# Kernel tuning notes

Measured on AMD Instinct MI355X. Metric: run time of the kernel, lower is better.

Reference implementation:

```python
import jax, jax.numpy as jnp
import numpy as np

B, T, D = 4, 2048, 1024  # batch, seq, latent_dim == attn_dim
H = 16                   # n_heads
HS = D // H              # head_size = 64
FF = 4 * D               # ffn hidden
EPS = 1e-5


def layernorm(x, g, b):
    mu = jnp.mean(x, axis=-1, keepdims=True)
    var = jnp.mean(jnp.square(x - mu), axis=-1, keepdims=True)
    return (x - mu) * jax.lax.rsqrt(var + EPS) * g + b


def setup_inputs() -> dict:
    key = jax.random.key(0)
    ks = jax.random.split(key, 12)
    s = lambda fan_in: 1.0 / np.sqrt(fan_in)
    return {
        "x": jax.random.normal(ks[0], (B, T, D), dtype=jnp.float32),
        "ln1_g": jnp.ones((D,), jnp.float32),
        "ln1_b": jnp.zeros((D,), jnp.float32),
        "W_ap": jax.random.normal(ks[1], (D, D), jnp.float32) * s(D),
        "b_ap": jnp.zeros((D,), jnp.float32),
        "W_qkv": jax.random.normal(ks[2], (D, 3 * D), jnp.float32) * s(D),
        "b_qkv": jnp.zeros((3 * D,), jnp.float32),
        "W_proj": jax.random.normal(ks[3], (D, D), jnp.float32) * s(D),
        "b_proj": jnp.zeros((D,), jnp.float32),
        "ln2_g": jnp.ones((D,), jnp.float32),
        "ln2_b": jnp.zeros((D,), jnp.float32),
        "W1": jax.random.normal(ks[4], (D, FF), jnp.float32) * s(D),
        "b1": jnp.zeros((FF,), jnp.float32),
        "W2": jax.random.normal(ks[5], (FF, D), jnp.float32) * s(FF),
        "b2": jnp.zeros((D,), jnp.float32),
    }


def block_fwd(x, ln1_g, ln1_b, W_ap, b_ap, W_qkv, b_qkv, W_proj, b_proj,
              ln2_g, ln2_b, W1, b1, W2, b2):
    # --- self attention branch ---
    a = layernorm(x, ln1_g, ln1_b)
    a = a @ W_ap + b_ap                       # [B,T,D]
    qkv = a @ W_qkv + b_qkv                   # [B,T,3D]
    q, k, v = jnp.split(qkv, 3, axis=-1)
    q = q.reshape(B, T, H, HS).transpose(0, 2, 1, 3)  # [B,H,T,HS]
    k = k.reshape(B, T, H, HS).transpose(0, 2, 1, 3)
    v = v.reshape(B, T, H, HS).transpose(0, 2, 1, 3)
    scores = jnp.einsum('bhqd,bhkd->bhqk', q, k) * (1.0 / np.sqrt(HS))
    probs = jax.nn.softmax(scores, axis=-1)   # full [B,H,T,T], no causal mask (as in source)
    o = jnp.einsum('bhqk,bhkd->bhqd', probs, v)
    o = o.transpose(0, 2, 1, 3).reshape(B, T, D)
    o = o @ W_proj + b_proj
    h = x + o
    # --- ffn branch: GELU(LayerNorm(h)) -> Linear -> GELU -> Linear ---
    f = jax.nn.gelu(layernorm(h, ln2_g, ln2_b), approximate=False)
    f = jax.nn.gelu(f @ W1 + b1, approximate=False) @ W2 + b2
    return h + f


def reference(x, ln1_g, ln1_b, W_ap, b_ap, W_qkv, b_qkv, W_proj, b_proj,
              ln2_g, ln2_b, W1, b1, W2, b2):
    return block_fwd(x, ln1_g, ln1_b, W_ap, b_ap, W_qkv, b_qkv, W_proj, b_proj,
                     ln2_g, ln2_b, W1, b1, W2, b2)
```

## Files before the change

### kernel.cpp

```cpp
#include <hip/hip_runtime.h>
#include <hip/hip_bf16.h>
#include <math.h>


typedef unsigned short u16;
typedef __attribute__((ext_vector_type(8))) short s16x8;
typedef __attribute__((ext_vector_type(4))) float f32x4;

__device__ __forceinline__ u16 f2bf(float f) {
    unsigned u = __float_as_uint(f);
    u += 0x7fffu + ((u >> 16) & 1u);
    return (u16)(u >> 16);
}
__device__ __forceinline__ unsigned pkbf2(float a, float b) {
    float2 t; t.x = a; t.y = b;
    __hip_bfloat162 r = __float22bfloat162_rn(t);
    return *(unsigned*)&r;
}
__device__ __forceinline__ float bf2f(short s) {
    return __uint_as_float(((unsigned)(unsigned short)s) << 16);
}
__device__ __forceinline__ float gelu_f(float v) {
    return 0.5f * v * (1.0f + erff(v * 0.70710678118654752f));
}

__global__ __launch_bounds__(256) void transpose_f32_bf16(
    const float* __restrict__ in, u16* __restrict__ out, int K, int N) {
    __shared__ float t[32][33];
    int n0 = blockIdx.x * 32, k0 = blockIdx.y * 32;
    int c = threadIdx.x, r0 = threadIdx.y;
#pragma unroll
    for (int i = 0; i < 4; i++) {
        int r = r0 + i * 8;
        t[r][c] = in[(size_t)(k0 + r) * N + n0 + c];
    }
    __syncthreads();
#pragma unroll
    for (int i = 0; i < 4; i++) {
        int r = r0 + i * 8;
        out[(size_t)(n0 + r) * K + k0 + c] = f2bf(t[c][r]);
    }
}

template <bool GELU>
__global__ __launch_bounds__(256) void ln_kernel(
    const float* __restrict__ x, const float* __restrict__ g,
    const float* __restrict__ bt, u16* __restrict__ out) {
    const int D = 1024;
    int row = blockIdx.x;
    float4 v = reinterpret_cast<const float4*>(x + (size_t)row * D)[threadIdx.x];
    float s = v.x + v.y + v.z + v.w;
    float s2 = v.x * v.x + v.y * v.y + v.z * v.z + v.w * v.w;
#pragma unroll
    for (int off = 32; off > 0; off >>= 1) {
        s += __shfl_down(s, off);
        s2 += __shfl_down(s2, off);
    }
    __shared__ float red[8];
    int wid = threadIdx.x >> 6;
    if ((threadIdx.x & 63) == 0) { red[wid] = s; red[wid + 4] = s2; }
    __syncthreads();
    s = red[0] + red[1] + red[2] + red[3];
    s2 = red[4] + red[5] + red[6] + red[7];
    float mu = s * (1.0f / 1024.0f);
    float var = s2 * (1.0f / 1024.0f) - mu * mu;
    float rstd = rsqrtf(var + 1e-5f);
    float4 gg = reinterpret_cast<const float4*>(g)[threadIdx.x];
    float4 bb = reinterpret_cast<const float4*>(bt)[threadIdx.x];
    float o0 = (v.x - mu) * rstd * gg.x + bb.x;
    float o1 = (v.y - mu) * rstd * gg.y + bb.y;
    float o2 = (v.z - mu) * rstd * gg.z + bb.z;
    float o3 = (v.w - mu) * rstd * gg.w + bb.w;
    if (GELU) { o0 = gelu_f(o0); o1 = gelu_f(o1); o2 = gelu_f(o2); o3 = gelu_f(o3); }
    uint2 o;
    o.x = pkbf2(o0, o1); o.y = pkbf2(o2, o3);
    reinterpret_cast<uint2*>(out + (size_t)row * D)[threadIdx.x] = o;
}

template <int OUT_BF16, int ACT_GELU, int HAS_RES, int SPLIT_V>
__global__ __launch_bounds__(256) void gemm_kernel(
    const u16* __restrict__ A, const u16* __restrict__ BT,
    const float* __restrict__ bias, const float* __restrict__ res,
    void* __restrict__ outp, u16* __restrict__ vtg, int M, int N, int K) {
    constexpr int LS = 72;
    __shared__ u16 As[128 * LS];
    __shared__ u16 Bs[128 * LS];
    const int m0 = blockIdx.y * 128, n0 = blockIdx.x * 128;
    const int tid = threadIdx.x;
    const int w = tid >> 6, lane = tid & 63, l16 = lane & 15, quad = lane >> 4;
    const int wm = (w >> 1) * 64, wn = (w & 1) * 64;

    const int r0 = tid >> 3;
    const int scol = (tid & 7) * 8;
    const u16* Ag = A + (size_t)(m0 + r0) * K + scol;
    const u16* Bg = BT + (size_t)(n0 + r0) * K + scol;

    s16x8 ra[4], rb[4];
#pragma unroll
    for (int c = 0; c < 4; c++) {
        ra[c] = *(const s16x8*)(Ag + (size_t)(c * 32) * K);
        rb[c] = *(const s16x8*)(Bg + (size_t)(c * 32) * K);
    }

    f32x4 acc[4][4] = {};

    for (int k0 = 0; k0 < K; k0 += 64) {
        __syncthreads();
#pragma unroll
        for (int c = 0; c < 4; c++) {
            *(s16x8*)&As[(c * 32 + r0) * LS + scol] = ra[c];
            *(s16x8*)&Bs[(c * 32 + r0) * LS + scol] = rb[c];
        }
        __syncthreads();
        if (k0 + 64 < K) {
#pragma unroll
            for (int c = 0; c < 4; c++) {
                ra[c] = *(const s16x8*)(Ag + (size_t)(c * 32) * K + k0 + 64);
                rb[c] = *(const s16x8*)(Bg + (size_t)(c * 32) * K + k0 + 64);
            }
        }
#pragma unroll
        for (int kd = 0; kd < 2; kd++) {
            s16x8 af[4], bf[4];
#pragma unroll
            for (int i = 0; i < 4; i++)
                af[i] = *(const s16x8*)&As[(wm + i * 16 + l16) * LS + kd * 32 + quad * 8];
#pragma unroll
            for (int j = 0; j < 4; j++)
                bf[j] = *(const s16x8*)&Bs[(wn + j * 16 + l16) * LS + kd * 32 + quad * 8];
#pragma unroll
            for (int i = 0; i < 4; i++)
#pragma unroll
                for (int j = 0; j < 4; j++)
                    acc[i][j] = __builtin_amdgcn_mfma_f32_16x16x32_bf16(
                        af[i], bf[j], acc[i][j], 0, 0, 0);
        }
    }

    float bv[4];
#pragma unroll
    for (int j = 0; j < 4; j++) bv[j] = bias[n0 + wn + j * 16 + l16];

    if (SPLIT_V && n0 >= 2048) {
#pragma unroll
        for (int i = 0; i < 4; i++) {
            int rowb = m0 + wm + i * 16 + quad * 4;
            int bb = rowb >> 11, tt = rowb & 2047;
#pragma unroll
            for (int j = 0; j < 4; j++) {
                int vcol = n0 + wn + j * 16 + l16 - 2048;
                uint2 pk;
                pk.x = pkbf2(acc[i][j][0] + bv[j], acc[i][j][1] + bv[j]);
                pk.y = pkbf2(acc[i][j][2] + bv[j], acc[i][j][3] + bv[j]);
                *(uint2*)&vtg[((size_t)bb * 1024 + vcol) * 2048 + tt] = pk;
            }
        }
    } else {
#pragma unroll
        for (int i = 0; i < 4; i++) {
            int rowb = m0 + wm + i * 16 + quad * 4;
#pragma unroll
            for (int j = 0; j < 4; j++) {
                int col = n0 + wn + j * 16 + l16;
#pragma unroll
                for (int r = 0; r < 4; r++) {
                    float v = acc[i][j][r] + bv[j];
                    if (ACT_GELU) v = gelu_f(v);
                    size_t idx = (size_t)(rowb + r) * N + col;
                    if (HAS_RES) v += res[idx];
                    if (OUT_BF16) ((u16*)outp)[idx] = f2bf(v);
                    else          ((float*)outp)[idx] = v;
                }
            }
        }
    }
}

__global__ __launch_bounds__(256) void knorm_kernel(
    const u16* __restrict__ qkv, float* __restrict__ maxkn) {
    const int T = 2048, D3 = 3072;
    int bh = blockIdx.x, b = bh >> 4, h = bh & 15;
    const u16* kg = qkv + (size_t)b * T * D3 + 1024 + h * 64;
    float mx = 0.f;
#pragma unroll
    for (int i = 0; i < 8; i++) {
        const u16* kp = kg + (size_t)(threadIdx.x + i * 256) * D3;
        float ss = 0.f;
#pragma unroll
        for (int c = 0; c < 8; c++) {
            s16x8 v = *(const s16x8*)(kp + c * 8);
#pragma unroll
            for (int j = 0; j < 8; j++) { float f = bf2f(v[j]); ss = fmaf(f, f, ss); }
        }
        mx = fmaxf(mx, ss);
    }
#pragma unroll
    for (int off = 32; off > 0; off >>= 1) mx = fmaxf(mx, __shfl_down(mx, off));
    __shared__ float red[4];
    if ((threadIdx.x & 63) == 0) red[threadIdx.x >> 6] = mx;
    __syncthreads();
    if (threadIdx.x == 0)
        maxkn[bh] = sqrtf(fmaxf(fmaxf(red[0], red[1]), fmaxf(red[2], red[3])));
}

__global__ __launch_bounds__(256, 4) void attn_kernel(
    const u16* __restrict__ qkv, const u16* __restrict__ vtg,
    const float* __restrict__ maxkn, u16* __restrict__ o) {
    const int T = 2048, D3 = 3072, Dm = 1024;
    const int bh = blockIdx.x, qb = blockIdx.y;
    const int b = bh >> 4, h = bh & 15;
    const int tid = threadIdx.x;
    const int w = tid >> 6, lane = tid & 63, l16 = lane & 15, quad = lane >> 4;
    const size_t tokbase = (size_t)b * T;
    const float s2 = 0.125f * 1.44269504088896f;

    __shared__ u16 Ks[64 * 72];
    __shared__ u16 Vts[64 * 72];
    __shared__ u16 Pt[4][32 * 72];

    s16x8 bq[2][2];
    float m2[2];
    const float kn = maxkn[bh];
#pragma unroll
    for (int qs = 0; qs < 2; qs++) {
        int qrow = qb * 128 + w * 32 + qs * 16 + l16;
        const u16* qp = qkv + (tokbase + qrow) * D3 + h * 64 + quad * 8;
        bq[qs][0] = *(const s16x8*)qp;
        bq[qs][1] = *(const s16x8*)(qp + 32);
        float ss = 0.f;
#pragma unroll
        for (int kd = 0; kd < 2; kd++)
#pragma unroll
            for (int j = 0; j < 8; j++) {
                float v = bf2f(bq[qs][kd][j]); ss = fmaf(v, v, ss);
            }
        ss += __shfl_xor(ss, 16);
        ss += __shfl_xor(ss, 32);
        m2[qs] = sqrtf(ss) * kn * s2;
    }

    f32x4 acc_ot[2][4] = {};
    float lp[2] = {0.f, 0.f};

    const u16* kgbase = qkv + tokbase * D3 + 1024 + h * 64;
    const u16* vgbase = vtg + ((size_t)b * 1024 + h * 64) * T;

    const int srow = tid >> 3;
    const int scv = (tid & 7) * 8;

    for (int kt = 0; kt < 32; kt++) {
        __syncthreads();
#pragma unroll
        for (int s = 0; s < 2; s++) {
            int row = srow + s * 32;
            *(s16x8*)&Ks[row * 72 + scv] =
                *(const s16x8*)(kgbase + (size_t)(kt * 64 + row) * D3 + scv);
            *(s16x8*)&Vts[row * 72 + scv] =
                *(const s16x8*)(vgbase + (size_t)row * T + kt * 64 + scv);
        }
        __syncthreads();

        f32x4 st[2][4] = {};
#pragma unroll
        for (int kd = 0; kd < 2; kd++)
#pragma unroll
            for (int kb = 0; kb < 4; kb++) {
                s16x8 ak = *(const s16x8*)&Ks[(kb * 16 + l16) * 72 + kd * 32 + quad * 8];
#pragma unroll
                for (int qs = 0; qs < 2; qs++)
                    st[qs][kb] = __builtin_amdgcn_mfma_f32_16x16x32_bf16(
                        ak, bq[qs][kd], st[qs][kb], 0, 0, 0);
            }

#pragma unroll
        for (int qs = 0; qs < 2; qs++) {
            float acc_l = 0.f;
#pragma unroll
            for (int kb = 0; kb < 4; kb++) {
#pragma unroll
                for (int r = 0; r < 4; r++) {
                    float pv = __builtin_amdgcn_exp2f(fmaf(st[qs][kb][r], s2, -m2[qs]));
                    st[qs][kb][r] = pv;
                    acc_l += pv;
                }
                uint2 pk;
                pk.x = pkbf2(st[qs][kb][0], st[qs][kb][1]);
                pk.y = pkbf2(st[qs][kb][2], st[qs][kb][3]);
                *(uint2*)&Pt[w][(qs * 16 + l16) * 72 + kb * 16 + quad * 4] = pk;
            }
            lp[qs] += acc_l;
        }

#pragma unroll
        for (int kk = 0; kk < 2; kk++) {
            s16x8 bp[2];
#pragma unroll
            for (int qs = 0; qs < 2; qs++)
                bp[qs] = *(const s16x8*)&Pt[w][(qs * 16 + l16) * 72 + kk * 32 + quad * 8];
#pragma unroll
            for (int dt = 0; dt < 4; dt++) {
                s16x8 av = *(const s16x8*)&Vts[(dt * 16 + l16) * 72 + kk * 32 + quad * 8];
#pragma unroll
                for (int qs = 0; qs < 2; qs++)
                    acc_ot[qs][dt] = __builtin_amdgcn_mfma_f32_16x16x32_bf16(
                        av, bp[qs], acc_ot[qs][dt], 0, 0, 0);
            }
        }
    }

#pragma unroll
    for (int qs = 0; qs < 2; qs++) {
        float l = lp[qs];
        l += __shfl_xor(l, 16);
        l += __shfl_xor(l, 32);
        float inv = 1.0f / l;
        int token = qb * 128 + w * 32 + qs * 16 + l16;
#pragma unroll
        for (int dt = 0; dt < 4; dt++) {
            uint2 pk;
            pk.x = pkbf2(acc_ot[qs][dt][0] * inv, acc_ot[qs][dt][1] * inv);
            pk.y = pkbf2(acc_ot[qs][dt][2] * inv, acc_ot[qs][dt][3] * inv);
            *(uint2*)&o[(tokbase + token) * Dm + h * 64 + dt * 16 + quad * 4] = pk;
        }
    }
}

extern "C" void kernel_launch(void* const* d_in, const int* in_sizes, int n_in,
                              void* d_out, int out_size, void* d_ws, size_t ws_size,
                              hipStream_t stream) {
    const int M = 8192;
    const int D = 1024, D3 = 3072, FF = 4096;

    const float* x      = (const float*)d_in[0];
    const float* ln1_g  = (const float*)d_in[1];
    const float* ln1_b  = (const float*)d_in[2];
    const float* W_ap   = (const float*)d_in[3];
    const float* b_ap   = (const float*)d_in[4];
    const float* W_qkv  = (const float*)d_in[5];
    const float* b_qkv  = (const float*)d_in[6];
    const float* W_proj = (const float*)d_in[7];
    const float* b_proj = (const float*)d_in[8];
    const float* ln2_g  = (const float*)d_in[9];
    const float* ln2_b  = (const float*)d_in[10];
    const float* W1     = (const float*)d_in[11];
    const float* b1     = (const float*)d_in[12];
    const float* W2     = (const float*)d_in[13];
    const float* b2     = (const float*)d_in[14];

    char* p = (char*)d_ws;
    auto carve = [&](size_t bytes) { char* r = p; p += (bytes + 255) & ~(size_t)255; return r; };
    u16*   WapT   = (u16*)carve((size_t)D * D * 2);
    u16*   WqkvT  = (u16*)carve((size_t)D * D3 * 2);
    u16*   WprojT = (u16*)carve((size_t)D * D * 2);
    u16*   W1T    = (u16*)carve((size_t)D * FF * 2);
    u16*   W2T    = (u16*)carve((size_t)FF * D * 2);
    u16*   aln    = (u16*)carve((size_t)M * D * 2);
    u16*   a1     = (u16*)carve((size_t)M * D * 2);
    u16*   qkvb   = (u16*)carve((size_t)M * D3 * 2);
    float* hbuf   = (float*)carve((size_t)M * D * 4);
    u16*   f1     = (u16*)carve((size_t)M * FF * 2);
    float* maxkn  = (float*)carve(64 * 4);
    u16* gbuf = aln;
    u16* obuf = a1;
    u16* vtg  = f1;

    dim3 tb(32, 8);
    transpose_f32_bf16<<<dim3(D / 32, D / 32), tb, 0, stream>>>(W_ap, WapT, D, D);
    transpose_f32_bf16<<<dim3(D3 / 32, D / 32), tb, 0, stream>>>(W_qkv, WqkvT, D, D3);
    transpose_f32_bf16<<<dim3(D / 32, D / 32), tb, 0, stream>>>(W_proj, WprojT, D, D);
    transpose_f32_bf16<<<dim3(FF / 32, D / 32), tb, 0, stream>>>(W1, W1T, D, FF);
    transpose_f32_bf16<<<dim3(D / 32, FF / 32), tb, 0, stream>>>(W2, W2T, FF, D);

    ln_kernel<false><<<M, 256, 0, stream>>>(x, ln1_g, ln1_b, aln);
    gemm_kernel<1, 0, 0, 0><<<dim3(D / 128, M / 128), 256, 0, stream>>>(
        aln, WapT, b_ap, nullptr, a1, nullptr, M, D, D);
    gemm_kernel<1, 0, 0, 1><<<dim3(D3 / 128, M / 128), 256, 0, stream>>>(
        a1, WqkvT, b_qkv, nullptr, qkvb, vtg, M, D3, D);
    knorm_kernel<<<64, 256, 0, stream>>>(qkvb, maxkn);
    attn_kernel<<<dim3(64, 16), 256, 0, stream>>>(qkvb, vtg, maxkn, obuf);
    gemm_kernel<0, 0, 1, 0><<<dim3(D / 128, M / 128), 256, 0, stream>>>(
        obuf, WprojT, b_proj, x, hbuf, nullptr, M, D, D);
    ln_kernel<true><<<M, 256, 0, stream>>>(hbuf, ln2_g, ln2_b, gbuf);
    gemm_kernel<1, 1, 0, 0><<<dim3(FF / 128, M / 128), 256, 0, stream>>>(
        gbuf, W1T, b1, nullptr, f1, nullptr, M, FF, D);
    gemm_kernel<0, 0, 1, 0><<<dim3(D / 128, M / 128), 256, 0, stream>>>(
        f1, W2T, b2, hbuf, (float*)d_out, nullptr, M, D, FF);
}
```

Before: 584.6 us.

## Load GEMM tiles directly to LDS with XOR swizzle; use tanh GELU

Swaps the register-staged, padded shared-memory tile loads in the GEMM for direct global-to-LDS loads on an unpadded, XOR-swizzled layout, with fragment reads un-swizzled to match. The aim is to cut VGPR staging and LDS store instructions, but it drops the register prefetch of the next k-tile, so global latency is no longer overlapped with MFMA work inside a block. It also replaces the exact erf GELU with a tanh approximation built from exp2 and rcp, which changes numerics relative to the exact reference.

```diff
diff --git a/kernel.cpp b/kernel.cpp
--- a/kernel.cpp
+++ b/kernel.cpp
@@ -21,7 +21,17 @@
     return __uint_as_float(((unsigned)(unsigned short)s) << 16);
 }
 __device__ __forceinline__ float gelu_f(float v) {
-    return 0.5f * v * (1.0f + erff(v * 0.70710678118654752f));
+    float u = v * v;
+    float x = v * fmaf(0.0356774081f, u, 0.7978845608f);
+    float t = __builtin_amdgcn_exp2f(x * 2.885390082f);
+    float th = fmaf(-2.0f, __builtin_amdgcn_rcpf(t + 1.0f), 1.0f);
+    float hv = 0.5f * v;
+    return fmaf(hv, th, hv);
+}
+__device__ __forceinline__ void glds16(const u16* g, u16* l) {
+    __builtin_amdgcn_global_load_lds(
+        (const __attribute__((address_space(1))) void*)g,
+        (__attribute__((address_space(3))) void*)l, 16, 0, 0);
 }
 
 __global__ __launch_bounds__(256) void transpose_f32_bf16(
@@ -82,52 +92,43 @@
     const u16* __restrict__ A, const u16* __restrict__ BT,
     const float* __restrict__ bias, const float* __restrict__ res,
     void* __restrict__ outp, u16* __restrict__ vtg, int M, int N, int K) {
-    constexpr int LS = 72;
-    __shared__ u16 As[128 * LS];
-    __shared__ u16 Bs[128 * LS];
+    __shared__ u16 As[128 * 64];
+    __shared__ u16 Bs[128 * 64];
     const int m0 = blockIdx.y * 128, n0 = blockIdx.x * 128;
     const int tid = threadIdx.x;
     const int w = tid >> 6, lane = tid & 63, l16 = lane & 15, quad = lane >> 4;
     const int wm = (w >> 1) * 64, wn = (w & 1) * 64;
 
-    const int r0 = tid >> 3;
-    const int scol = (tid & 7) * 8;
-    const u16* Ag = A + (size_t)(m0 + r0) * K + scol;
-    const u16* Bg = BT + (size_t)(n0 + r0) * K + scol;
-
-    s16x8 ra[4], rb[4];
-#pragma unroll
-    for (int c = 0; c < 4; c++) {
-        ra[c] = *(const s16x8*)(Ag + (size_t)(c * 32) * K);
-        rb[c] = *(const s16x8*)(Bg + (size_t)(c * 32) * K);
-    }
+    const int lrow = lane >> 3;
+    const int lcol = ((lane & 7) ^ lrow) * 8;
+    const u16* Ag = A + (size_t)(m0 + w * 32 + lrow) * K + lcol;
+    const u16* Bg = BT + (size_t)(n0 + w * 32 + lrow) * K + lcol;
+    u16* Asl = &As[(w * 32) * 64];
+    u16* Bsl = &Bs[(w * 32) * 64];
 
     f32x4 acc[4][4] = {};
 
     for (int k0 = 0; k0 < K; k0 += 64) {
         __syncthreads();
 #pragma unroll
-        for (int c = 0; c < 4; c++) {
-            *(s16x8*)&As[(c * 32 + r0) * LS + scol] = ra[c];
-            *(s16x8*)&Bs[(c * 32 + r0) * LS + scol] = rb[c];
+        for (int j = 0; j < 4; j++) {
+            glds16(Ag + k0 + (size_t)(j * 8) * K, Asl + j * 8 * 64);
+            glds16(Bg + k0 + (size_t)(j * 8) * K, Bsl + j * 8 * 64);
         }
         __syncthreads();
-        if (k0 + 64 < K) {
-#pragma unroll
-            for (int c = 0; c < 4; c++) {
-                ra[c] = *(const s16x8*)(Ag + (size_t)(c * 32) * K + k0 + 64);
-                rb[c] = *(const s16x8*)(Bg + (size_t)(c * 32) * K + k0 + 64);
-            }
-        }
 #pragma unroll
         for (int kd = 0; kd < 2; kd++) {
             s16x8 af[4], bf[4];
 #pragma unroll
-            for (int i = 0; i < 4; i++)
-                af[i] = *(const s16x8*)&As[(wm + i * 16 + l16) * LS + kd * 32 + quad * 8];
-#pragma unroll
-            for (int j = 0; j < 4; j++)
-                bf[j] = *(const s16x8*)&Bs[(wn + j * 16 + l16) * LS + kd * 32 + quad * 8];
+            for (int i = 0; i < 4; i++) {
+                int r = wm + i * 16 + l16;
+                af[i] = *(const s16x8*)&As[r * 64 + ((kd * 4 + quad) ^ (lane & 7)) * 8];
+            }
+#pragma unroll
+            for (int j = 0; j < 4; j++) {
+                int r = wn + j * 16 + l16;
+                bf[j] = *(const s16x8*)&Bs[r * 64 + ((kd * 4 + quad) ^ (lane & 7)) * 8];
+            }
 #pragma unroll
             for (int i = 0; i < 4; i++)
 #pragma unroll
```

Measured after the change: 571.1 us. 1.02x faster.
